# Optimization experiments

Measured on AMD Instinct MI355X. Metric: run time of the kernel, lower is better.

The kernel has to match this reference:

```python
import jax, jax.numpy as jnp
import numpy as np

D_STATE = 16
DT_RANK = 48
D_CONV = 4
EPS = 1e-5


def rmsnorm(x, w):
    return x * jax.lax.rsqrt(jnp.mean(x * x, axis=-1, keepdims=True) + EPS) * w


def causal_dw_conv(u, w, b):
    # u: [B,T,D], w: [D,K] depthwise causal kernel, b: [D]
    B, T, D = u.shape
    K = w.shape[1]
    up = jnp.pad(u, ((0, 0), (K - 1, 0), (0, 0)))
    acc = jnp.zeros_like(u)
    for k in range(K):  # K=4, tiny fixed loop
        acc = acc + up[:, k:k + T, :] * w[:, k]
    return acc + b


def mamba_mixer(h, ipw, cw, cb, xpw, dpw, dpb, alog, dpar, opw):
    # h: [B,T,d_model]
    B, T, _ = h.shape
    xz = h @ ipw.T                       # [B,T,2*d_inner]
    u, z = jnp.split(xz, 2, axis=-1)     # each [B,T,d_inner]
    u = jax.nn.silu(causal_dw_conv(u, cw, cb))
    xp = u @ xpw.T                       # [B,T,dt_rank+2*d_state]
    dt = xp[..., :DT_RANK]
    Bm = xp[..., DT_RANK:DT_RANK + D_STATE]
    Cm = xp[..., DT_RANK + D_STATE:]
    delta = jax.nn.softplus(dt @ dpw.T + dpb)      # [B,T,d_inner]
    A = -jnp.exp(alog)                              # [d_inner, d_state], negative
    dA = jnp.exp(delta[..., None] * A)              # [B,T,d_inner,d_state] in (0,1)
    dBu = (delta * u)[..., None] * Bm[:, :, None, :]
    # time-major for scan
    dA_t = jnp.moveaxis(dA, 1, 0)
    dBu_t = jnp.moveaxis(dBu, 1, 0)
    C_t = jnp.moveaxis(Cm, 1, 0)

    def step(hst, inp):
        a, bu, c = inp
        hst = a * hst + bu                          # [B,d_inner,d_state]
        y = jnp.einsum('bdn,bn->bd', hst, c)
        return hst, y

    h0 = jnp.zeros((B, u.shape[-1], D_STATE), u.dtype)
    _, ys = jax.lax.scan(step, h0, (dA_t, dBu_t, C_t))
    y = jnp.moveaxis(ys, 0, 1) + u * dpar           # skip via D
    y = y * jax.nn.silu(z)                          # gate
    return y @ opw.T                                # [B,T,d_model]


def setup_inputs() -> dict:
    key = jax.random.key(0)
    ks = jax.random.split(key, 16)
    L, d_model, d_inner = 4, 768, 1536
    B, C, T = 4, 256, 512
    s = 0.02
    return {
        'x': jax.random.normal(ks[0], (B, C, T), jnp.float32),
        'in_proj_w': jax.random.normal(ks[1], (L, 2 * d_inner, d_model), jnp.float32) * s,
        'conv_w': jax.random.normal(ks[2], (L, d_inner, D_CONV), jnp.float32) * 0.3,
        'conv_b': jnp.zeros((L, d_inner), jnp.float32),
        'x_proj_w': jax.random.normal(ks[3], (L, DT_RANK + 2 * D_STATE, d_inner), jnp.float32) * s,
        'dt_proj_w': jax.random.normal(ks[4], (L, d_inner, DT_RANK), jnp.float32) * 0.1,
        'dt_proj_b': jax.random.normal(ks[5], (L, d_inner), jnp.float32) * 0.1 - 4.0,
        'A_log': jax.random.uniform(ks[6], (L, d_inner, D_STATE), jnp.float32, 0.0, 1.5),
        'D_param': jax.random.uniform(ks[7], (L, d_inner), jnp.float32),
        'out_proj_w': jax.random.normal(ks[8], (L, d_model, d_inner), jnp.float32) * s,
        'norm_w': jnp.ones((L, d_model), jnp.float32),
        'norm_f_w': jnp.ones((d_model,), jnp.float32),
        'inp_w': jax.random.normal(ks[9], (d_model, C), jnp.float32) * s,
        'inp_b': jnp.zeros((d_model,), jnp.float32),
        'cls_w': jax.random.normal(ks[10], (10, d_model), jnp.float32) * s,
        'cls_b': jnp.zeros((10,), jnp.float32),
    }


def reference(x, in_proj_w, conv_w, conv_b, x_proj_w, dt_proj_w, dt_proj_b,
              A_log, D_param, out_proj_w, norm_w, norm_f_w,
              inp_w, inp_b, cls_w, cls_b):
    # x: (B, C, T) -> (B, T, C)
    xt = jnp.transpose(x, (0, 2, 1))
    h = xt @ inp_w.T + inp_b                # [B,T,d_model]
    hidden = h
    residual = None
    L = in_proj_w.shape[0]
    for l in range(L):
        residual = hidden if residual is None else hidden + residual
        normed = rmsnorm(residual, norm_w[l])
        hidden = mamba_mixer(normed, in_proj_w[l], conv_w[l], conv_b[l],
                             x_proj_w[l], dt_proj_w[l], dt_proj_b[l],
                             A_log[l], D_param[l], out_proj_w[l])
    residual = hidden + residual
    hidden = rmsnorm(residual, norm_f_w)
    pooled = hidden.mean(axis=1)            # [B,d_model]
    logits = pooled @ cls_w.T + cls_b       # [B,num_labels]
    return logits
```

## Files before the change

### kernel.cpp

```cpp
#include <hip/hip_runtime.h>
#include <math.h>

#define D_MODEL 768
#define D_INNER 1536
#define B_SZ 4
#define T_SZ 512
#define ROWS (B_SZ*T_SZ)
#define XP_N 80
#define CH 16
#define CT 32
#define XS 8
#define XKC (D_INNER/XS)
#define OS 2
#define OKC (D_INNER/OS)
#define MN_OUT (ROWS*768)

typedef __attribute__((ext_vector_type(8))) short bf16x8;
typedef __attribute__((ext_vector_type(4))) float f32x4;

#define GLL(g, l) __builtin_amdgcn_global_load_lds( \
    (const __attribute__((address_space(1))) void*)(g), \
    (__attribute__((address_space(3))) void*)(l), 16, 0, 0)

__device__ __forceinline__ float sigmoidf_(float x){ return 1.0f/(1.0f+__expf(-x)); }
__device__ __forceinline__ float siluf_(float x){ return x*sigmoidf_(x); }
__device__ __forceinline__ unsigned short f2bf(float f){
  unsigned u = __builtin_bit_cast(unsigned, f);
  u = (u + 0x7FFFu + ((u >> 16) & 1u)) >> 16;
  return (unsigned short)u;
}

__global__ __launch_bounds__(256) void gemm_bf16(
    const unsigned short* __restrict__ A, const unsigned short* __restrict__ Wb,
    float* __restrict__ C, int M, int N, int K)
{
  __shared__ unsigned short As[2][64*32];
  __shared__ unsigned short Ws[2][128*32];
  const int tid = threadIdx.x;
  const int bm = blockIdx.y*64, bn = blockIdx.x*128;
  const int wave = tid >> 6, lane = tid & 63;
  const int wn = wave*32;
  const int fr = lane & 15, quad = lane >> 4;
  f32x4 acc[4][2] = {};
  const int chunk = wave*64 + lane;
  const int row0 = chunk >> 2;
  const int khp  = chunk & 3;
  const int khl  = (khp + 4 - ((row0 >> 1) & 3)) & 3;
  const unsigned short* Ag = A  + (size_t)(bm + row0)*K + khl*8;
  const unsigned short* Wg = Wb + (size_t)(bn + row0)*K + khl*8;
  const size_t rstep = (size_t)64*K;
  const int wo = wave*512;

  GLL(Ag,         As[0] + wo);
  GLL(Wg,         Ws[0] + wo);
  GLL(Wg + rstep, Ws[0] + wo + 2048);
  asm volatile("s_waitcnt vmcnt(0)" ::: "memory");
  __builtin_amdgcn_sched_barrier(0);
  __builtin_amdgcn_s_barrier();

  int cur = 0;
  for (int k0 = 0; k0 < K; k0 += 32){
    const int nxt = cur ^ 1;
    if (k0 + 32 < K){
      GLL(Ag + k0 + 32,         As[nxt] + wo);
      GLL(Wg + k0 + 32,         Ws[nxt] + wo);
      GLL(Wg + rstep + k0 + 32, Ws[nxt] + wo + 2048);
    }
    bf16x8 a[4], b[2];
    #pragma unroll
    for (int i=0;i<4;i++){
      const int row = i*16 + fr;
      a[i] = *(const bf16x8*)(As[cur] + row*32 + (((quad + (row>>1)) & 3)*8));
    }
    #pragma unroll
    for (int j=0;j<2;j++){
      const int row = wn + j*16 + fr;
      b[j] = *(const bf16x8*)(Ws[cur] + row*32 + (((quad + (row>>1)) & 3)*8));
    }
    #pragma unroll
    for (int i=0;i<4;i++)
      #pragma unroll
      for (int j=0;j<2;j++)
        acc[i][j] = __builtin_amdgcn_mfma_f32_16x16x32_bf16(a[i], b[j], acc[i][j], 0, 0, 0);
    asm volatile("s_waitcnt vmcnt(0)" ::: "memory");
    __builtin_amdgcn_sched_barrier(0);
    __builtin_amdgcn_s_barrier();
    cur = nxt;
  }
  #pragma unroll
  for (int i=0;i<4;i++){
    #pragma unroll
    for (int r=0;r<4;r++){
      const int row = bm + i*16 + quad*4 + r;
      float* Cp = C + (size_t)row*N + bn + wn + fr;
      #pragma unroll
      for (int j=0;j<2;j++)
        Cp[j*16] = acc[i][j][r];
    }
  }
}

__global__ __launch_bounds__(256) void gemm_bf16_sk(
    const unsigned short* __restrict__ A, const unsigned short* __restrict__ Wb,
    float* __restrict__ P0, float* __restrict__ P1, int M, int N, int K)
{
  __shared__ unsigned short As[2][64*32];
  __shared__ unsigned short Ws[2][128*32];
  const int tid = threadIdx.x;
  const int bm = blockIdx.y*64, bn = blockIdx.x*128;
  const int s = blockIdx.z;
  const int koff = s*OKC;
  const int wave = tid >> 6, lane = tid & 63;
  const int wn = wave*32;
  const int fr = lane & 15, quad = lane >> 4;
  f32x4 acc[4][2] = {};
  const int chunk = wave*64 + lane;
  const int row0 = chunk >> 2;
  const int khp  = chunk & 3;
  const int khl  = (khp + 4 - ((row0 >> 1) & 3)) & 3;
  const unsigned short* Ag = A  + (size_t)(bm + row0)*K + koff + khl*8;
  const unsigned short* Wg = Wb + (size_t)(bn + row0)*K + koff + khl*8;
  const size_t rstep = (size_t)64*K;
  const int wo = wave*512;

  GLL(Ag,         As[0] + wo);
  GLL(Wg,         Ws[0] + wo);
  GLL(Wg + rstep, Ws[0] + wo + 2048);
  asm volatile("s_waitcnt vmcnt(0)" ::: "memory");
  __builtin_amdgcn_sched_barrier(0);
  __builtin_amdgcn_s_barrier();

  int cur = 0;
  for (int k0 = 0; k0 < OKC; k0 += 32){
    const int nxt = cur ^ 1;
    if (k0 + 32 < OKC){
      GLL(Ag + k0 + 32,         As[nxt] + wo);
      GLL(Wg + k0 + 32,         Ws[nxt] + wo);
      GLL(Wg + rstep + k0 + 32, Ws[nxt] + wo + 2048);
    }
    bf16x8 a[4], b[2];
    #pragma unroll
    for (int i=0;i<4;i++){
      const int row = i*16 + fr;
      a[i] = *(const bf16x8*)(As[cur] + row*32 + (((quad + (row>>1)) & 3)*8));
    }
    #pragma unroll
    for (int j=0;j<2;j++){
      const int row = wn + j*16 + fr;
      b[j] = *(const bf16x8*)(Ws[cur] + row*32 + (((quad + (row>>1)) & 3)*8));
    }
    #pragma unroll
    for (int i=0;i<4;i++)
      #pragma unroll
      for (int j=0;j<2;j++)
        acc[i][j] = __builtin_amdgcn_mfma_f32_16x16x32_bf16(a[i], b[j], acc[i][j], 0, 0, 0);
    asm volatile("s_waitcnt vmcnt(0)" ::: "memory");
    __builtin_amdgcn_sched_barrier(0);
    __builtin_amdgcn_s_barrier();
    cur = nxt;
  }
  float* Cb = (s == 0 ? P0 : P1);
  #pragma unroll
  for (int i=0;i<4;i++){
    #pragma unroll
    for (int r=0;r<4;r++){
      const int row = bm + i*16 + quad*4 + r;
      float* Cp = Cb + (size_t)row*N + bn + wn + fr;
      #pragma unroll
      for (int j=0;j<2;j++)
        Cp[j*16] = acc[i][j][r];
    }
  }
}

__global__ __launch_bounds__(256) void sgemm_input(
    const float* __restrict__ x, const float* __restrict__ W,
    const float* __restrict__ bias, float* __restrict__ C)
{
  __shared__ float As[16][64];
  __shared__ float Wsh[16][64];
  const int bm = blockIdx.y*64, bn = blockIdx.x*64;
  const int b = bm >> 9, t0 = bm & (T_SZ-1);
  const int tid = threadIdx.x;
  const int tx = tid & 15, ty = tid >> 4;
  const int lm = tid & 63, lk = (tid >> 6) << 2;
  float acc[4][4] = {};
  const float* Wp = W + (size_t)(bn+lm)*256 + lk;
  const float* xb = x + ((size_t)b*256)*512 + t0 + lm;
  for (int k0 = 0; k0 < 256; k0 += 16){
    #pragma unroll
    for (int i=0;i<4;i++)
      As[lk+i][lm] = xb[(size_t)(k0+lk+i)*512];
    float4 wv = *(const float4*)(Wp + k0);
    Wsh[lk+0][lm]=wv.x; Wsh[lk+1][lm]=wv.y; Wsh[lk+2][lm]=wv.z; Wsh[lk+3][lm]=wv.w;
    __syncthreads();
    #pragma unroll
    for (int k = 0; k < 16; k++){
      float a[4], w[4];
      #pragma unroll
      for (int i=0;i<4;i++) a[i] = As[k][ty*4+i];
      #pragma unroll
      for (int j=0;j<4;j++) w[j] = Wsh[k][tx*4+j];
      #pragma unroll
      for (int i=0;i<4;i++)
        #pragma unroll
        for (int j=0;j<4;j++)
          acc[i][j] += a[i]*w[j];
    }
    __syncthreads();
  }
  #pragma unroll
  for (int i=0;i<4;i++){
    const int r = bm + ty*4 + i;
    #pragma unroll
    for (int j=0;j<4;j++){
      const int n = bn + tx*4 + j;
      C[(size_t)r*768 + n] = acc[i][j] + bias[n];
    }
  }
}

__global__ __launch_bounds__(256) void xproj_conv_splitk(
    const float* __restrict__ xz, const float* __restrict__ cw,
    const float* __restrict__ cb, const float* __restrict__ W,
    float* __restrict__ part)
{
  __shared__ float As[16][64];
  __shared__ float Wsh[16][80];
  const int bm = blockIdx.x*64;
  const int s = blockIdx.y;
  const int koff = s*XKC;
  const int tid = threadIdx.x;
  const int tx = tid & 15, ty = tid >> 4;
  const int lm = tid & 63, lk = (tid >> 6) << 2;
  float acc[4][5] = {};
  const int row = bm + lm;
  const int t = row & (T_SZ-1);
  for (int k0 = 0; k0 < XKC; k0 += 16){
    const int d0 = koff + k0 + lk;
    float4 cbv = *(const float4*)(cb + d0);
    float cba[4] = {cbv.x, cbv.y, cbv.z, cbv.w};
    float4 tp3 = *(const float4*)(xz + (size_t)row*3072 + d0);
    float4 tp0 = (t>=3) ? *(const float4*)(xz + (size_t)(row-3)*3072 + d0) : make_float4(0.f,0.f,0.f,0.f);
    float4 tp1 = (t>=2) ? *(const float4*)(xz + (size_t)(row-2)*3072 + d0) : make_float4(0.f,0.f,0.f,0.f);
    float4 tp2 = (t>=1) ? *(const float4*)(xz + (size_t)(row-1)*3072 + d0) : make_float4(0.f,0.f,0.f,0.f);
    float a0[4]={tp0.x,tp0.y,tp0.z,tp0.w}, a1[4]={tp1.x,tp1.y,tp1.z,tp1.w};
    float a2[4]={tp2.x,tp2.y,tp2.z,tp2.w}, a3[4]={tp3.x,tp3.y,tp3.z,tp3.w};
    #pragma unroll
    for (int i=0;i<4;i++){
      const float4 w4 = *(const float4*)(cw + (size_t)(d0+i)*4);
      float a = cba[i];
      a += a0[i]*w4.x; a += a1[i]*w4.y; a += a2[i]*w4.z; a += a3[i]*w4.w;
      As[lk+i][lm] = siluf_(a);
    }
    for (int i = tid; i < 320; i += 256){
      const int wr = i % 80, wk = (i / 80) << 2;
      float4 wv = *(const float4*)(W + (size_t)wr*D_INNER + koff + k0 + wk);
      Wsh[wk+0][wr]=wv.x; Wsh[wk+1][wr]=wv.y; Wsh[wk+2][wr]=wv.z; Wsh[wk+3][wr]=wv.w;
    }
    __syncthreads();
    #pragma unroll
    for (int k = 0; k < 16; k++){
      float a[4], w[5];
      #pragma unroll
      for (int i=0;i<4;i++) a[i] = As[k][ty*4+i];
      #pragma unroll
      for (int j=0;j<5;j++) w[j] = Wsh[k][tx*5+j];
      #pragma unroll
      for (int i=0;i<4;i++)
        #pragma unroll
        for (int j=0;j<5;j++)
          acc[i][j] += a[i]*w[j];
    }
    __syncthreads();
  }
  #pragma unroll
  for (int i=0;i<4;i++){
    const int r = bm + ty*4 + i;
    #pragma unroll
    for (int j=0;j<5;j++){
      const int n = tx*5 + j;
      part[((size_t)s*ROWS + r)*XP_N + n] = acc[i][j];
    }
  }
}

__global__ __launch_bounds__(256) void dtproj_fused(
    const float* __restrict__ part, const float* __restrict__ W,
    const float* __restrict__ bias, float* __restrict__ delta,
    float* __restrict__ xpbc)
{
  if (blockIdx.x >= 24){
    const int i = ((blockIdx.x - 24)*32 + blockIdx.y)*256 + threadIdx.x;
    const int r = i >> 5, cc = i & 31;
    float ssum = 0.f;
    #pragma unroll
    for (int s2=0;s2<XS;s2++)
      ssum += part[((size_t)s2*ROWS + r)*XP_N + 48 + cc];
    xpbc[(size_t)r*32 + cc] = ssum;
    return;
  }
  __shared__ float As[16][64];
  __shared__ float Wsh[16][64];
  const int bm = blockIdx.y*64, bn = blockIdx.x*64;
  const int tid = threadIdx.x;
  const int tx = tid & 15, ty = tid >> 4;
  const int lm = tid & 63, lk = (tid >> 6) << 2;
  float acc[4][4] = {};
  const float* Ap = part + (size_t)(bm+lm)*XP_N + lk;
  const float* Wp = W + (size_t)(bn+lm)*48 + lk;
  for (int k0 = 0; k0 < 48; k0 += 16){
    float4 av = make_float4(0.f,0.f,0.f,0.f);
    #pragma unroll
    for (int s2=0;s2<XS;s2++){
      const float4 pv = *(const float4*)(Ap + (size_t)s2*ROWS*XP_N + k0);
      av.x += pv.x; av.y += pv.y; av.z += pv.z; av.w += pv.w;
    }
    float4 wv = *(const float4*)(Wp + k0);
    As[lk+0][lm]=av.x; As[lk+1][lm]=av.y; As[lk+2][lm]=av.z; As[lk+3][lm]=av.w;
    Wsh[lk+0][lm]=wv.x; Wsh[lk+1][lm]=wv.y; Wsh[lk+2][lm]=wv.z; Wsh[lk+3][lm]=wv.w;
    __syncthreads();
    #pragma unroll
    for (int k = 0; k < 16; k++){
      float a[4], w[4];
      #pragma unroll
      for (int i=0;i<4;i++) a[i] = As[k][ty*4+i];
      #pragma unroll
      for (int j=0;j<4;j++) w[j] = Wsh[k][tx*4+j];
      #pragma unroll
      for (int i=0;i<4;i++)
        #pragma unroll
        for (int j=0;j<4;j++)
          acc[i][j] += a[i]*w[j];
    }
    __syncthreads();
  }
  #pragma unroll
  for (int i=0;i<4;i++){
    const int r = bm + ty*4 + i;
    #pragma unroll
    for (int j=0;j<4;j++){
      const int n = bn + tx*4 + j;
      float v = acc[i][j] + bias[n];
      v = (v > 20.f) ? v : log1pf(__expf(v));
      delta[(size_t)r*D_INNER + n] = v;
    }
  }
}

__global__ __launch_bounds__(256) void scan_pass1(
    const float* __restrict__ delta, const float* __restrict__ xz,
    const float* __restrict__ xpbc, const float* __restrict__ alog,
    const float* __restrict__ cw, const float* __restrict__ cb,
    float* __restrict__ sdvp, float* __restrict__ Hend)
{
  const int d = blockIdx.x*256 + threadIdx.x;
  const int b = blockIdx.y, c = blockIdx.z;
  float4 t0 = *(const float4*)(alog + d*16 + 0);
  float4 t1 = *(const float4*)(alog + d*16 + 4);
  float4 t2 = *(const float4*)(alog + d*16 + 8);
  float4 t3 = *(const float4*)(alog + d*16 + 12);
  float Av[16] = {t0.x,t0.y,t0.z,t0.w,t1.x,t1.y,t1.z,t1.w,
                  t2.x,t2.y,t2.z,t2.w,t3.x,t3.y,t3.z,t3.w};
  float h[16];
  #pragma unroll
  for (int n=0;n<16;n++){ Av[n] = -__expf(Av[n]); h[n]=0.f; }
  float sdv = 0.f;
  const size_t row0 = (size_t)b*T_SZ + (size_t)c*CT;
  const float* dp  = delta + row0*D_INNER + d;
  const float* xp0 = xz    + row0*3072 + d;
  const float* bp  = xpbc  + row0*32;
  const float4 cwv = *(const float4*)(cw + (size_t)d*4);
  const float cbv = cb[d];
  float xm3, xm2, xm1;
  if (c == 0){ xm3 = xm2 = xm1 = 0.f; }
  else { xm3 = xp0[-3*3072]; xm2 = xp0[-2*3072]; xm1 = xp0[-1*3072]; }
  #pragma unroll 4
  for (int tt=0; tt<CT; tt++){
    const float dv = dp[(size_t)tt*D_INNER];
    const float xc = xp0[(size_t)tt*3072];
    float ua = cbv;
    ua += xm3*cwv.x; ua += xm2*cwv.y; ua += xm1*cwv.z; ua += xc*cwv.w;
    const float uv = siluf_(ua);
    xm3 = xm2; xm2 = xm1; xm1 = xc;
    const float4 B0 = *(const float4*)(bp + (size_t)tt*32);
    const float4 B1 = *(const float4*)(bp + (size_t)tt*32 + 4);
    const float4 B2 = *(const float4*)(bp + (size_t)tt*32 + 8);
    const float4 B3 = *(const float4*)(bp + (size_t)tt*32 + 12);
    const float Bv[16] = {B0.x,B0.y,B0.z,B0.w,B1.x,B1.y,B1.z,B1.w,
                          B2.x,B2.y,B2.z,B2.w,B3.x,B3.y,B3.z,B3.w};
    const float du = dv*uv;
    sdv += dv;
    #pragma unroll
    for (int n=0;n<16;n++){
      const float dA = __expf(dv*Av[n]);
      h[n] = dA*h[n] + du*Bv[n];
    }
  }
  sdvp[(size_t)(b*CH+c)*D_INNER + d] = sdv;
  float* Hp = Hend + ((size_t)(b*CH+c)*D_INNER + d)*16;
  *(float4*)(Hp+ 0) = make_float4(h[0],h[1],h[2],h[3]);
  *(float4*)(Hp+ 4) = make_float4(h[4],h[5],h[6],h[7]);
  *(float4*)(Hp+ 8) = make_float4(h[8],h[9],h[10],h[11]);
  *(float4*)(Hp+12) = make_float4(h[12],h[13],h[14],h[15]);
}

__global__ __launch_bounds__(256) void scan_combine(
    const float* __restrict__ sdvp, const float* __restrict__ Hend,
    const float* __restrict__ alog, float* __restrict__ Hin)
{
  const int gid = blockIdx.x*256 + threadIdx.x;
  const int b = gid / (D_INNER*16);
  const int r = gid % (D_INNER*16);
  const int d = r >> 4;
  const float Av = -__expf(alog[r]);
  const size_t baseh = (size_t)b*CH*D_INNER*16 + r;
  const size_t steph = (size_t)D_INNER*16;
  const size_t bases = (size_t)b*CH*D_INNER + d;
  const size_t steps = (size_t)D_INNER;
  float h = 0.f;
  Hin[baseh] = 0.f;
  #pragma unroll
  for (int c=0; c<CH-1; c++){
    const float P = __expf(Av * sdvp[bases + (size_t)c*steps]);
    h = P*h + Hend[baseh + (size_t)c*steph];
    Hin[baseh + (size_t)(c+1)*steph] = h;
  }
}

__global__ __launch_bounds__(256) void scan_pass3(
    const float* __restrict__ delta, const float* __restrict__ xz,
    const float* __restrict__ xpbc, const float* __restrict__ alog,
    const float* __restrict__ cw, const float* __restrict__ cb,
    const float* __restrict__ Dp, const float* __restrict__ Hin,
    unsigned short* __restrict__ yb)
{
  const int d = blockIdx.x*256 + threadIdx.x;
  const int b = blockIdx.y, c = blockIdx.z;
  float4 t0 = *(const float4*)(alog + d*16 + 0);
  float4 t1 = *(const float4*)(alog + d*16 + 4);
  float4 t2 = *(const float4*)(alog + d*16 + 8);
  float4 t3 = *(const float4*)(alog + d*16 + 12);
  float Av[16] = {t0.x,t0.y,t0.z,t0.w,t1.x,t1.y,t1.z,t1.w,
                  t2.x,t2.y,t2.z,t2.w,t3.x,t3.y,t3.z,t3.w};
  #pragma unroll
  for (int n=0;n<16;n++) Av[n] = -__expf(Av[n]);
  const float* Hp = Hin + ((size_t)(b*CH+c)*D_INNER + d)*16;
  float4 h0 = *(const float4*)(Hp+0);
  float4 h1 = *(const float4*)(Hp+4);
  float4 h2 = *(const float4*)(Hp+8);
  float4 h3 = *(const float4*)(Hp+12);
  float h[16] = {h0.x,h0.y,h0.z,h0.w,h1.x,h1.y,h1.z,h1.w,
                 h2.x,h2.y,h2.z,h2.w,h3.x,h3.y,h3.z,h3.w};
  const float Dv = Dp[d];
  const size_t row0 = (size_t)b*T_SZ + (size_t)c*CT;
  const float* dp  = delta + row0*D_INNER + d;
  const float* xp0 = xz    + row0*3072 + d;
  const float* zp  = xz    + row0*3072 + 1536 + d;
  const float* bp  = xpbc  + row0*32;
  unsigned short* yp = yb + row0*D_INNER + d;
  const float4 cwv = *(const float4*)(cw + (size_t)d*4);
  const float cbv = cb[d];
  float xm3, xm2, xm1;
  if (c == 0){ xm3 = xm2 = xm1 = 0.f; }
  else { xm3 = xp0[-3*3072]; xm2 = xp0[-2*3072]; xm1 = xp0[-1*3072]; }
  #pragma unroll 2
  for (int tt=0; tt<CT; tt++){
    const float dv = dp[(size_t)tt*D_INNER];
    const float xc = xp0[(size_t)tt*3072];
    const float zv = zp[(size_t)tt*3072];
    float ua = cbv;
    ua += xm3*cwv.x; ua += xm2*cwv.y; ua += xm1*cwv.z; ua += xc*cwv.w;
    const float uv = siluf_(ua);
    xm3 = xm2; xm2 = xm1; xm1 = xc;
    const float4 B0 = *(const float4*)(bp + (size_t)tt*32);
    const float4 B1 = *(const float4*)(bp + (size_t)tt*32 + 4);
    const float4 B2 = *(const float4*)(bp + (size_t)tt*32 + 8);
    const float4 B3 = *(const float4*)(bp + (size_t)tt*32 + 12);
    const float4 C0 = *(const float4*)(bp + (size_t)tt*32 + 16);
    const float4 C1 = *(const float4*)(bp + (size_t)tt*32 + 20);
    const float4 C2 = *(const float4*)(bp + (size_t)tt*32 + 24);
    const float4 C3 = *(const float4*)(bp + (size_t)tt*32 + 28);
    const float Bv[16] = {B0.x,B0.y,B0.z,B0.w,B1.x,B1.y,B1.z,B1.w,
                          B2.x,B2.y,B2.z,B2.w,B3.x,B3.y,B3.z,B3.w};
    const float Cv[16] = {C0.x,C0.y,C0.z,C0.w,C1.x,C1.y,C1.z,C1.w,
                          C2.x,C2.y,C2.z,C2.w,C3.x,C3.y,C3.z,C3.w};
    const float du = dv*uv;
    float pp = 0.f;
    #pragma unroll
    for (int n=0;n<16;n++){
      const float dA = __expf(dv*Av[n]);
      h[n] = dA*h[n] + du*Bv[n];
      pp += h[n]*Cv[n];
    }
    yp[(size_t)tt*D_INNER] = f2bf((pp + uv*Dv)*siluf_(zv));
  }
}

__global__ __launch_bounds__(256) void fused_norm_cast(
    float* __restrict__ resid, const float* __restrict__ P0, const float* __restrict__ P1,
    const float* __restrict__ w, unsigned short* __restrict__ obf, float* __restrict__ ofp,
    const float* __restrict__ cin1, unsigned short* __restrict__ co1, int cn1, int cnb1,
    const float* __restrict__ cin2, unsigned short* __restrict__ co2, int cn2)
{
  const int blk = blockIdx.x;
  if (blk >= 2048){
    const int cb = blk - 2048;
    const float* in; unsigned short* o; int i4;
    if (cb < cnb1){ in = cin1; o = co1; i4 = (cb*256 + threadIdx.x)*4; if (i4 >= cn1) return; }
    else { in = cin2; o = co2; i4 = ((cb-cnb1)*256 + threadIdx.x)*4; if (i4 >= cn2) return; }
    float4 v = *(const float4*)(in + i4);
    ushort4 r;
    r.x = f2bf(v.x); r.y = f2bf(v.y); r.z = f2bf(v.z); r.w = f2bf(v.w);
    *(ushort4*)(o + i4) = r;
    return;
  }
  const int row = blk;
  const int tid = threadIdx.x;
  float v[3];
  float ss = 0.f;
  #pragma unroll
  for (int i=0;i<3;i++){
    const int c = tid + i*256;
    const size_t idx = (size_t)row*768 + c;
    float r = resid[idx];
    if (P0) r += P0[idx] + P1[idx];
    v[i] = r;
    ss += r*r;
  }
  #pragma unroll
  for (int off=32; off>=1; off>>=1) ss += __shfl_xor(ss, off);
  __shared__ float sred[4];
  const int lane = tid & 63, wv = tid >> 6;
  if (lane == 0) sred[wv] = ss;
  __syncthreads();
  const float tot = sred[0]+sred[1]+sred[2]+sred[3];
  const float scale = rsqrtf(tot*(1.0f/768.0f) + 1e-5f);
  #pragma unroll
  for (int i=0;i<3;i++){
    const int c = tid + i*256;
    const size_t idx = (size_t)row*768 + c;
    if (P0) resid[idx] = v[i];
    const float o = v[i]*scale*w[c];
    if (obf) obf[idx] = f2bf(o);
    else     ofp[idx] = o;
  }
}

__global__ __launch_bounds__(256) void pool_partial(const float* __restrict__ normed,
                                                    float* __restrict__ part){
  const int i = blockIdx.x*256 + threadIdx.x;
  const int s = blockIdx.y;
  const int b = i / 768, m = i % 768;
  float sum = 0.f;
  const float* p = normed + ((size_t)b*T_SZ + s*32)*768 + m;
  #pragma unroll
  for (int t=0; t<32; t++) sum += p[(size_t)t*768];
  part[s*3072 + i] = sum;
}

__global__ __launch_bounds__(256) void pool_cls(const float* __restrict__ part,
                                                const float* __restrict__ cw,
                                                const float* __restrict__ cb,
                                                float* __restrict__ out){
  __shared__ float ls[768];
  const int b = blockIdx.x;
  const int tid = threadIdx.x;
  #pragma unroll
  for (int i=0;i<3;i++){
    const int m = tid + i*256;
    float s = 0.f;
    #pragma unroll
    for (int c=0;c<16;c++) s += part[c*3072 + b*768 + m];
    ls[m] = s * (1.0f/T_SZ);
  }
  __syncthreads();
  const int wave = tid >> 6, lane = tid & 63;
  for (int o = wave; o < 10; o += 4){
    float s = 0.f;
    for (int k = lane; k < 768; k += 64) s += ls[k]*cw[o*768 + k];
    #pragma unroll
    for (int off=32; off>=1; off>>=1) s += __shfl_xor(s, off);
    if (lane == 0) out[b*10 + o] = s + cb[o];
  }
}

extern "C" void kernel_launch(void* const* d_in, const int* in_sizes, int n_in,
                              void* d_out, int out_size, void* d_ws, size_t ws_size,
                              hipStream_t stream) {
  const float* x         = (const float*)d_in[0];
  const float* in_proj_w = (const float*)d_in[1];
  const float* conv_w    = (const float*)d_in[2];
  const float* conv_b    = (const float*)d_in[3];
  const float* x_proj_w  = (const float*)d_in[4];
  const float* dt_proj_w = (const float*)d_in[5];
  const float* dt_proj_b = (const float*)d_in[6];
  const float* A_log     = (const float*)d_in[7];
  const float* D_param   = (const float*)d_in[8];
  const float* out_proj_w= (const float*)d_in[9];
  const float* norm_w    = (const float*)d_in[10];
  const float* norm_f_w  = (const float*)d_in[11];
  const float* inp_w     = (const float*)d_in[12];
  const float* inp_b     = (const float*)d_in[13];
  const float* cls_w     = (const float*)d_in[14];
  const float* cls_b     = (const float*)d_in[15];
  float* out = (float*)d_out;

  char* ws = (char*)d_ws;
  auto carve = [&](size_t nelem)->float* {
    float* p = (float*)ws;
    ws += ((nelem*sizeof(float) + 255)/256)*256;
    return p;
  };
  float* resid  = carve((size_t)ROWS*768);
  float* normed = carve((size_t)ROWS*768);
  float* xz     = carve((size_t)ROWS*3072);
  float* ucv    = carve((size_t)ROWS*1536);
  float* xpbc   = carve((size_t)ROWS*32);
  float* delta  = carve((size_t)ROWS*1536);
  float* ybf_f  = carve((size_t)ROWS*1536/2);
  float* wbi_f  = carve((size_t)(3072*768)/2);
  float* wbo_f  = carve((size_t)(768*1536)/2);
  float* sdvbuf = carve((size_t)B_SZ*CH*D_INNER);
  float* Hend   = carve((size_t)B_SZ*CH*D_INNER*16);
  float* Hin    = carve((size_t)B_SZ*CH*D_INNER*16);
  float* xpart  = carve((size_t)XS*ROWS*XP_N);
  float* ppool  = carve((size_t)16*3072);

  unsigned short* normedb = (unsigned short*)normed;
  unsigned short* ybf = (unsigned short*)ybf_f;
  unsigned short* wbi = (unsigned short*)wbi_f;
  unsigned short* wbo = (unsigned short*)wbo_f;

  sgemm_input<<<dim3(12,32), 256, 0, stream>>>(x, inp_w, inp_b, resid);

  for (int l = 0; l < 4; l++){
    fused_norm_cast<<<2048 + 2304 + 1152, 256, 0, stream>>>(
        resid, l ? delta : nullptr, l ? ucv : nullptr,
        norm_w + (size_t)l*768, normedb, nullptr,
        in_proj_w + (size_t)l*3072*768, wbi, 3072*768, 2304,
        out_proj_w + (size_t)l*768*1536, wbo, 768*1536);
    gemm_bf16<<<dim3(24,32), 256, 0, stream>>>(normedb, wbi, xz, ROWS, 3072, 768);
    xproj_conv_splitk<<<dim3(32,XS), 256, 0, stream>>>(
        xz, conv_w + (size_t)l*1536*4, conv_b + (size_t)l*1536,
        x_proj_w + (size_t)l*XP_N*1536, xpart);
    dtproj_fused<<<dim3(32,32), 256, 0, stream>>>(
        xpart, dt_proj_w + (size_t)l*1536*48, dt_proj_b + (size_t)l*1536, delta, xpbc);
    scan_pass1<<<dim3(6,B_SZ,CH-1), 256, 0, stream>>>(
        delta, xz, xpbc, A_log + (size_t)l*1536*16,
        conv_w + (size_t)l*1536*4, conv_b + (size_t)l*1536, sdvbuf, Hend);
    scan_combine<<<(B_SZ*D_INNER*16)/256, 256, 0, stream>>>(
        sdvbuf, Hend, A_log + (size_t)l*1536*16, Hin);
    scan_pass3<<<dim3(6,B_SZ,CH), 256, 0, stream>>>(
        delta, xz, xpbc, A_log + (size_t)l*1536*16,
        conv_w + (size_t)l*1536*4, conv_b + (size_t)l*1536,
        D_param + (size_t)l*1536, Hin, ybf);
    gemm_bf16_sk<<<dim3(6,32,OS), 256, 0, stream>>>(ybf, wbo, delta, ucv, ROWS, 768, 1536);
  }

  fused_norm_cast<<<2048, 256, 0, stream>>>(
      resid, delta, ucv, norm_f_w, nullptr, normed,
      nullptr, nullptr, 0, 0, nullptr, nullptr, 0);
  pool_partial<<<dim3(12,16), 256, 0, stream>>>(normed, ppool);
  pool_cls<<<4, 256, 0, stream>>>(ppool, cls_w, cls_b, out);
}
```

Baseline: 821.2 us.

## Fold chunk-state combine into scan pass3 and double the chunk count

The separate scan_combine kernel and its Hin buffer are removed. Each pass3 block now rebuilds its starting state by serially folding all earlier chunks' end states and delta sums. Chunk count goes from 16 to 32 with 16 timesteps per chunk, which doubles parallelism in pass1 and pass3. The cost is redundant work in pass3: later chunks re-read and recombine up to 31 prior states, so the combine work grows quadratically in chunk count.

```diff
diff --git a/kernel.cpp b/kernel.cpp
--- a/kernel.cpp
+++ b/kernel.cpp
@@ -7,8 +7,8 @@
 #define T_SZ 512
 #define ROWS (B_SZ*T_SZ)
 #define XP_N 80
-#define CH 16
-#define CT 32
+#define CH 32
+#define CT 16
 #define XS 8
 #define XKC (D_INNER/XS)
 #define OS 2
@@ -405,35 +405,12 @@
   *(float4*)(Hp+12) = make_float4(h[12],h[13],h[14],h[15]);
 }
 
-__global__ __launch_bounds__(256) void scan_combine(
-    const float* __restrict__ sdvp, const float* __restrict__ Hend,
-    const float* __restrict__ alog, float* __restrict__ Hin)
-{
-  const int gid = blockIdx.x*256 + threadIdx.x;
-  const int b = gid / (D_INNER*16);
-  const int r = gid % (D_INNER*16);
-  const int d = r >> 4;
-  const float Av = -__expf(alog[r]);
-  const size_t baseh = (size_t)b*CH*D_INNER*16 + r;
-  const size_t steph = (size_t)D_INNER*16;
-  const size_t bases = (size_t)b*CH*D_INNER + d;
-  const size_t steps = (size_t)D_INNER;
-  float h = 0.f;
-  Hin[baseh] = 0.f;
-  #pragma unroll
-  for (int c=0; c<CH-1; c++){
-    const float P = __expf(Av * sdvp[bases + (size_t)c*steps]);
-    h = P*h + Hend[baseh + (size_t)c*steph];
-    Hin[baseh + (size_t)(c+1)*steph] = h;
-  }
-}
-
 __global__ __launch_bounds__(256) void scan_pass3(
     const float* __restrict__ delta, const float* __restrict__ xz,
     const float* __restrict__ xpbc, const float* __restrict__ alog,
     const float* __restrict__ cw, const float* __restrict__ cb,
-    const float* __restrict__ Dp, const float* __restrict__ Hin,
-    unsigned short* __restrict__ yb)
+    const float* __restrict__ Dp, const float* __restrict__ sdvp,
+    const float* __restrict__ Hend, unsigned short* __restrict__ yb)
 {
   const int d = blockIdx.x*256 + threadIdx.x;
   const int b = blockIdx.y, c = blockIdx.z;
@@ -445,13 +422,25 @@
                   t2.x,t2.y,t2.z,t2.w,t3.x,t3.y,t3.z,t3.w};
   #pragma unroll
   for (int n=0;n<16;n++) Av[n] = -__expf(Av[n]);
-  const float* Hp = Hin + ((size_t)(b*CH+c)*D_INNER + d)*16;
-  float4 h0 = *(const float4*)(Hp+0);
-  float4 h1 = *(const float4*)(Hp+4);
-  float4 h2 = *(const float4*)(Hp+8);
-  float4 h3 = *(const float4*)(Hp+12);
-  float h[16] = {h0.x,h0.y,h0.z,h0.w,h1.x,h1.y,h1.z,h1.w,
-                 h2.x,h2.y,h2.z,h2.w,h3.x,h3.y,h3.z,h3.w};
+  float h[16];
+  #pragma unroll
+  for (int n=0;n<16;n++) h[n] = 0.f;
+  {
+    const size_t bases = (size_t)b*CH*D_INNER + d;
+    for (int j = 0; j < c; j++){
+      const float sdv = sdvp[bases + (size_t)j*D_INNER];
+      const float* Hj = Hend + (bases + (size_t)j*D_INNER)*16;
+      const float4 H0 = *(const float4*)(Hj+0);
+      const float4 H1 = *(const float4*)(Hj+4);
+      const float4 H2 = *(const float4*)(Hj+8);
+      const float4 H3 = *(const float4*)(Hj+12);
+      const float Hv[16] = {H0.x,H0.y,H0.z,H0.w,H1.x,H1.y,H1.z,H1.w,
+                            H2.x,H2.y,H2.z,H2.w,H3.x,H3.y,H3.z,H3.w};
+      #pragma unroll
+      for (int n=0;n<16;n++)
+        h[n] = __expf(Av[n]*sdv)*h[n] + Hv[n];
+    }
+  }
   const float Dv = Dp[d];
   const size_t row0 = (size_t)b*T_SZ + (size_t)c*CT;
   const float* dp  = delta + row0*D_INNER + d;
@@ -623,7 +612,6 @@
   float* wbo_f  = carve((size_t)(768*1536)/2);
   float* sdvbuf = carve((size_t)B_SZ*CH*D_INNER);
   float* Hend   = carve((size_t)B_SZ*CH*D_INNER*16);
-  float* Hin    = carve((size_t)B_SZ*CH*D_INNER*16);
   float* xpart  = carve((size_t)XS*ROWS*XP_N);
   float* ppool  = carve((size_t)16*3072);
 
@@ -649,12 +637,10 @@
     scan_pass1<<<dim3(6,B_SZ,CH-1), 256, 0, stream>>>(
         delta, xz, xpbc, A_log + (size_t)l*1536*16,
         conv_w + (size_t)l*1536*4, conv_b + (size_t)l*1536, sdvbuf, Hend);
-    scan_combine<<<(B_SZ*D_INNER*16)/256, 256, 0, stream>>>(
-        sdvbuf, Hend, A_log + (size_t)l*1536*16, Hin);
     scan_pass3<<<dim3(6,B_SZ,CH), 256, 0, stream>>>(
         delta, xz, xpbc, A_log + (size_t)l*1536*16,
         conv_w + (size_t)l*1536*4, conv_b + (size_t)l*1536,
-        D_param + (size_t)l*1536, Hin, ybf);
+        D_param + (size_t)l*1536, sdvbuf, Hend, ybf);
     gemm_bf16_sk<<<dim3(6,32,OS), 256, 0, stream>>>(ybf, wbo, delta, ucv, ROWS, 768, 1536);
   }
 
```

Result: no change. 819.0 us (-0.3%).
